# Kernel optimization log

Hardware: AMD Instinct MI355X
Metric: run time of the kernel (lower is better)

## Reference

```python
import jax, jax.numpy as jnp
import numpy as np

EPS = 1e-6

def setup_inputs() -> dict:
    key = jax.random.key(0)
    ks = jax.random.split(key, 8)
    S, B, I, D, L = 1024, 16, 1024, 1024, 2
    std = np.sqrt(2.0 / (5.0 * I))
    inp = {
        "input": jax.random.normal(ks[0], (S, B, I), jnp.float32),
        "h0": jnp.zeros((L, B, D), jnp.float32),
        "extra0": jnp.zeros((L, B, 3 * D), jnp.float32),
        "W0": jax.random.normal(ks[1], (4 * D, I), jnp.float32) * std,
        "b0": jnp.zeros((4 * D,), jnp.float32).at[2 * D:3 * D].set(
            jax.random.uniform(ks[2], (D,), jnp.float32, 3.0, 6.0)),
        "r0": jnp.zeros((4 * D,), jnp.float32),
        "W1": jax.random.normal(ks[3], (4 * D, D), jnp.float32) * std,
        "b1": jnp.zeros((4 * D,), jnp.float32).at[2 * D:3 * D].set(
            jax.random.uniform(ks[4], (D,), jnp.float32, 3.0, 6.0)),
        "r1": jnp.zeros((4 * D,), jnp.float32),
    }
    return inp

def _cell(x, c, n, h, m, W, b, r):
    # x: (B, in), states: (B, D), W: (4D, in), b/r: (4D,)
    D = h.shape[-1]
    pre = x @ W.T + b  # (B, 4D)
    rz, ri, rf, ro = jnp.split(r, 4)
    z_pre = pre[:, 0 * D:1 * D] + rz * h
    i_pre = pre[:, 1 * D:2 * D] + ri * h
    f_pre = pre[:, 2 * D:3 * D] + rf * h
    o_pre = pre[:, 3 * D:4 * D] + ro * h
    z_t = jnp.tanh(z_pre)
    o_t = jax.nn.sigmoid(o_pre)
    m_new = jnp.maximum(f_pre + m, i_pre)
    f_t = jnp.exp(f_pre + m - m_new)
    i_t = jnp.exp(i_pre - m_new)
    c_new = f_t * c + i_t * z_t
    n_new = f_t * n + i_t
    h_new = o_t * (c_new / (jnp.abs(n_new) + EPS))
    return h_new, c_new, n_new, m_new

def _run(input, h0, extra0, params):
    D = h0.shape[-1]
    c0 = extra0[:, :, 0 * D:1 * D]
    n0 = extra0[:, :, 1 * D:2 * D]
    m0 = extra0[:, :, 2 * D:3 * D]

    def step(carry, x_t):
        h, c, n, m = carry  # each (L, B, D)
        x = x_t
        hs, cs, ns, ms = [], [], [], []
        for l, (W, b, r) in enumerate(params):
            h_new, c_new, n_new, m_new = _cell(x, c[l], n[l], h[l], m[l], W, b, r)
            hs.append(h_new); cs.append(c_new); ns.append(n_new); ms.append(m_new)
            x = h_new
        carry = (jnp.stack(hs), jnp.stack(cs), jnp.stack(ns), jnp.stack(ms))
        return carry, x

    (h_f, c_f, n_f, m_f), output = jax.lax.scan(step, (h0, c0, n0, m0), input)
    extra_f = jnp.concatenate([c_f, n_f, m_f], axis=-1)
    return output, h_f, extra_f

def reference(input, h0, extra0, W0, b0, r0, W1, b1, r1):
    params = [(W0, b0, r0), (W1, b1, r1)]
    return _run(input, h0, extra0, params)
```

## Files before the change

### kernel.cpp

```cpp
#include <hip/hip_runtime.h>
#include <hip/hip_bf16.h>

#define S_LEN  1024
#define BATCH  16
#define IDIM   1024
#define DDIM   1024
#define NG     4096
#define BD     16384
#define LAYERS 2
#define PF     16

typedef __attribute__((ext_vector_type(8))) short   short8;
typedef __attribute__((ext_vector_type(4))) float   floatx4;
typedef __attribute__((address_space(1))) void      as1_void;
typedef __attribute__((address_space(3))) void      as3_void;

#define L2E  1.4426950408889634f
#define LN2  0.6931471805599453f

#define EXP2F(x) exp2f(x)

static __device__ __forceinline__ unsigned short f2bf(float x) {
    unsigned int u = __float_as_uint(x);
    return (unsigned short)((u + 0x7fffu + ((u >> 16) & 1u)) >> 16);
}

__global__ void detect_dtype(const void* w, int* flag)
{
    const __hip_bfloat16* p = (const __hip_bfloat16*)w;
    float mx = 0.0f;
    for (int i = threadIdx.x; i < 4096; i += 64) {
        float v = __bfloat162float(p[i]);
        float a = fabsf(v);
        if (!(a == a)) a = 1e30f;
        mx = fmaxf(mx, a);
    }
#pragma unroll
    for (int o = 32; o > 0; o >>= 1)
        mx = fmaxf(mx, __shfl_down(mx, o, 64));
    if (threadIdx.x == 0) *flag = (mx > 1e3f) ? 1 : 0;
}

__global__ void detect_rzero(const float* __restrict__ pb, int* __restrict__ rflag)
{
    const float* r = pb + (size_t)(1 + 2 * blockIdx.x) * NG;
    int nz = 0;
    for (int i = threadIdx.x; i < NG; i += 256) nz |= (r[i] != 0.0f);
    __shared__ int s[4];
    const int w = threadIdx.x >> 6;
    const int any = __any(nz) ? 1 : 0;
    if ((threadIdx.x & 63) == 0) s[w] = any;
    __syncthreads();
    if (threadIdx.x == 0) rflag[blockIdx.x] = !(s[0] | s[1] | s[2] | s[3]);
}

__global__ void to_bf16(const void* src, size_t elem_off, const int* flag,
                        unsigned short* dst, int n)
{
    const int i = blockIdx.x * 256 + threadIdx.x;
    if (i >= n) return;
    if (*flag) dst[i] = f2bf(((const float*)src)[elem_off + i]);
    else       dst[i] = ((const unsigned short*)src)[elem_off + i];
}

__global__ void to_f32(const void* src, const int* flag, float* dst, int n)
{
    const int i = blockIdx.x * 256 + threadIdx.x;
    if (i >= n) return;
    dst[i] = (*flag) ? ((const float*)src)[i]
                     : __bfloat162float(((const __hip_bfloat16*)src)[i]);
}

__global__ __launch_bounds__(256, 2)
void gemm_bias(const __hip_bfloat16* __restrict__ A,
               const __hip_bfloat16* __restrict__ W,
               const float* __restrict__ bias,
               unsigned short* __restrict__ out,
               const int* __restrict__ rflag)
{
    constexpr int K = 1024;
    __shared__ alignas(16) __hip_bfloat16 sA[128 * 32];
    __shared__ alignas(16) __hip_bfloat16 sB[128 * 32];

    const int t  = threadIdx.x;
    const int m0 = blockIdx.y * 128;
    const int nb = blockIdx.x;
    const int lr = t & 15;
    const int q  = (t >> 4) & 3;
    const int w  = t >> 6;
    const int wm = w >> 1, wn = w & 1;
    const int sr = t >> 2;
    const int qd = t & 3;
    const int qs = qd ^ ((sr >> 1) & 3);

    floatx4 acc[4][4] = {};

    const __hip_bfloat16* Ab = A + (size_t)(m0 + sr) * K + qs * 8;
    const int wrow = ((sr >> 5) << 10) + nb * 32 + (sr & 31);
    const __hip_bfloat16* Wb = W + (size_t)wrow * K + qs * 8;

    const int rc = (q ^ ((lr >> 1) & 3)) * 8;

    for (int k0 = 0; k0 < K; k0 += 32) {
        __syncthreads();
        __builtin_amdgcn_global_load_lds((as1_void*)(Ab + k0),            (as3_void*)&sA[sr * 32 + qd * 8],        16, 0, 0);
        __builtin_amdgcn_global_load_lds((as1_void*)(Ab + 64 * K + k0),   (as3_void*)&sA[(sr + 64) * 32 + qd * 8], 16, 0, 0);
        __builtin_amdgcn_global_load_lds((as1_void*)(Wb + k0),            (as3_void*)&sB[sr * 32 + qd * 8],        16, 0, 0);
        __builtin_amdgcn_global_load_lds((as1_void*)(Wb + 2048 * K + k0), (as3_void*)&sB[(sr + 64) * 32 + qd * 8], 16, 0, 0);
        __syncthreads();

        short8 af[4], bf[4];
#pragma unroll
        for (int i = 0; i < 4; i++)
            af[i] = *(const short8*)&sA[(wm * 64 + i * 16 + lr) * 32 + rc];
#pragma unroll
        for (int j = 0; j < 4; j++)
            bf[j] = *(const short8*)&sB[(j * 32 + wn * 16 + lr) * 32 + rc];
#pragma unroll
        for (int i = 0; i < 4; i++)
#pragma unroll
            for (int j = 0; j < 4; j++)
                acc[i][j] = __builtin_amdgcn_mfma_f32_16x16x32_bf16(af[i], bf[j], acc[i][j], 0, 0, 0);
    }

    const int d = nb * 32 + wn * 16 + lr;
    const float sc[4] = {2.0f * L2E, L2E, L2E, L2E};
    float bb[4];
#pragma unroll
    for (int g = 0; g < 4; g++) bb[g] = sc[g] * bias[g * 1024 + d];

    const int rfast = *rflag;

#pragma unroll
    for (int i = 0; i < 4; i++) {
#pragma unroll
        for (int reg = 0; reg < 4; reg++) {
            const int row = m0 + wm * 64 + i * 16 + q * 4 + reg;
            float v[4];
#pragma unroll
            for (int g = 0; g < 4; g++)
                v[g] = acc[i][g][reg] * sc[g] + bb[g];
            if (rfast) {
                const float zv = v[0];
                const float e2 = EXP2F(-fabsf(zv));
                v[0] = copysignf((1.0f - e2) * __builtin_amdgcn_rcpf(1.0f + e2), zv);
                v[3] = __builtin_amdgcn_rcpf(1.0f + EXP2F(-v[3]));
            }
            union { unsigned short us[4]; uint2 u2; } pk;
#pragma unroll
            for (int g = 0; g < 4; g++) pk.us[g] = f2bf(v[g]);
            *(uint2*)(out + (size_t)row * NG + d * 4) = pk.u2;
        }
    }
}

template<int MODE>
__global__ void slstm_scan(const unsigned int* __restrict__ pre,
                           const float* __restrict__ r,
                           float* __restrict__ state,
                           unsigned short* __restrict__ hseq,
                           void* __restrict__ gout, size_t gout_eoff,
                           const int* __restrict__ flag,
                           const int* __restrict__ rflag, int T)
{
    const int idx = blockIdx.x * 64 + threadIdx.x;
    const int b = idx >> 10;
    const int d = idx & 1023;
    const int fl = *flag;
    const int rfast = *rflag;

    const float rz = r[d]            * (2.0f * L2E);
    const float ri = r[DDIM + d]     * L2E;
    const float rf = r[2 * DDIM + d] * L2E;
    const float ro = r[3 * DDIM + d] * L2E;

    float c  = state[0 * BD + idx];
    float n  = state[1 * BD + idx];
    float m2 = state[2 * BD + idx];
    float h  = state[3 * BD + idx];

    const size_t stp = 32768;
    const unsigned int* p = pre + (size_t)b * 2048 + (size_t)d * 2;

    unsigned short* hb = hseq + (size_t)b * DDIM + d;
    float*          fo = (float*)gout + gout_eoff + (size_t)b * DDIM + d;
    unsigned short* bo = (unsigned short*)gout + gout_eoff + (size_t)b * DDIM + d;

    unsigned int k0[PF], k1[PF];
#pragma unroll
    for (int u = 0; u < PF; u++) {
        const uint2 v = *(const uint2*)(p + (size_t)u * stp);
        k0[u] = v.x; k1[u] = v.y;
    }

    if (rfast) {
        for (int t8 = 0; t8 < T; t8 += PF) {
#pragma unroll
            for (int u = 0; u < PF; u++) {
                const float zt = __uint_as_float(k0[u] << 16);
                const float i2 = __uint_as_float(k0[u] & 0xffff0000u);
                const float f2 = __uint_as_float(k1[u] << 16);
                const float ot = __uint_as_float(k1[u] & 0xffff0000u);

                const uint2 nv = *(const uint2*)(p + (size_t)(t8 + u + PF) * stp);
                k0[u] = nv.x; k1[u] = nv.y;

                const float fm = f2 + m2;
                const float mn = fmaxf(fm, i2);
                const float ft = EXP2F(fm - mn);
                const float it = EXP2F(i2 - mn);

                c  = fmaf(ft, c, it * zt);
                n  = fmaf(ft, n, it);
                m2 = mn;
                h  = ot * c * __builtin_amdgcn_rcpf(fabsf(n) + 1e-6f);

                const size_t toff = (size_t)(t8 + u) * BD;
                if (MODE == 0)      hb[toff] = f2bf(h);
                else if (fl)        fo[toff] = h;
                else                bo[toff] = f2bf(h);
            }
        }
    } else {
        for (int t8 = 0; t8 < T; t8 += PF) {
#pragma unroll
            for (int u = 0; u < PF; u++) {
                float z2 = __uint_as_float(k0[u] << 16);
                float i2 = __uint_as_float(k0[u] & 0xffff0000u);
                float f2 = __uint_as_float(k1[u] << 16);
                float o2 = __uint_as_float(k1[u] & 0xffff0000u);

                const uint2 nv = *(const uint2*)(p + (size_t)(t8 + u + PF) * stp);
                k0[u] = nv.x; k1[u] = nv.y;

                z2 = fmaf(rz, h, z2);
                i2 = fmaf(ri, h, i2);
                f2 = fmaf(rf, h, f2);
                o2 = fmaf(ro, h, o2);

                const float fm = f2 + m2;
                const float mn = fmaxf(fm, i2);
                const float ft = EXP2F(fm - mn);
                const float it = EXP2F(i2 - mn);

                const float e2 = EXP2F(-fabsf(z2));
                const float zt = copysignf((1.0f - e2) * __builtin_amdgcn_rcpf(1.0f + e2), z2);
                const float ot = __builtin_amdgcn_rcpf(1.0f + EXP2F(-o2));

                c  = ft * c + it * zt;
                n  = ft * n + it;
                m2 = mn;
                h  = ot * c * __builtin_amdgcn_rcpf(fabsf(n) + 1e-6f);

                const size_t toff = (size_t)(t8 + u) * BD;
                if (MODE == 0)      hb[toff] = f2bf(h);
                else if (fl)        fo[toff] = h;
                else                bo[toff] = f2bf(h);
            }
        }
    }

    state[0 * BD + idx] = c;
    state[1 * BD + idx] = n;
    state[2 * BD + idx] = m2;
    state[3 * BD + idx] = h;
}

__global__ void init_state(const void* __restrict__ h0,
                           const void* __restrict__ extra0,
                           const int* __restrict__ flag,
                           float* __restrict__ state)
{
    const int idx = blockIdx.x * 256 + threadIdx.x;
    const int l  = idx / BD;
    const int bd = idx % BD;
    const int b = bd >> 10, d = bd & 1023;
    float* st = state + (size_t)l * 4 * BD;
    const size_t eoff = ((size_t)l * BATCH + b) * (3 * DDIM);
    float cv, nv, mv, hv;
    if (*flag) {
        const float* e = (const float*)extra0 + eoff;
        cv = e[d]; nv = e[DDIM + d]; mv = e[2 * DDIM + d];
        hv = ((const float*)h0)[(size_t)l * BD + bd];
    } else {
        const __hip_bfloat16* e = (const __hip_bfloat16*)extra0 + eoff;
        cv = __bfloat162float(e[d]);
        nv = __bfloat162float(e[DDIM + d]);
        mv = __bfloat162float(e[2 * DDIM + d]);
        hv = __bfloat162float(((const __hip_bfloat16*)h0)[(size_t)l * BD + bd]);
    }
    st[0 * BD + bd] = cv;
    st[1 * BD + bd] = nv;
    st[2 * BD + bd] = mv * L2E;
    st[3 * BD + bd] = hv;
}

__global__ void finalize(const float* __restrict__ state,
                         void* __restrict__ out,
                         const int* __restrict__ flag)
{
    const int idx = blockIdx.x * 256 + threadIdx.x;
    const int l  = idx / BD;
    const int bd = idx % BD;
    const int b = bd >> 10, d = bd & 1023;
    const float* st = state + (size_t)l * 4 * BD;
    const float cv = st[0 * BD + bd], nv = st[1 * BD + bd];
    const float mv = st[2 * BD + bd] * LN2;
    const float hv = st[3 * BD + bd];

    const size_t hoff = (size_t)S_LEN * BD + idx;
    const size_t eoff = (size_t)S_LEN * BD + (size_t)LAYERS * BD
                      + ((size_t)l * BATCH + b) * (3 * DDIM);
    if (*flag) {
        float* o = (float*)out;
        o[hoff] = hv;
        o[eoff + d] = cv; o[eoff + DDIM + d] = nv; o[eoff + 2 * DDIM + d] = mv;
    } else {
        unsigned short* o = (unsigned short*)out;
        o[hoff] = f2bf(hv);
        o[eoff + d]            = f2bf(cv);
        o[eoff + DDIM + d]     = f2bf(nv);
        o[eoff + 2 * DDIM + d] = f2bf(mv);
    }
}

__global__ void zero_out_k(void* __restrict__ out, const int* __restrict__ flag,
                           int out_size)
{
    const size_t i = (size_t)blockIdx.x * 256 + threadIdx.x;
    const size_t nb = (size_t)out_size * ((*flag) ? 4 : 2);
    char* o = (char*)out;
    for (size_t j = i * 4; j < (i + 1) * 4 && j < nb; j++) o[j] = 0;
}

extern "C" void kernel_launch(void* const* d_in, const int* in_sizes, int n_in,
                              void* d_out, int out_size, void* d_ws, size_t ws_size,
                              hipStream_t stream)
{
    const void* input  = d_in[0];
    const void* h0     = d_in[1];
    const void* extra0 = d_in[2];
    const void* W0     = d_in[3];
    const void* b0     = d_in[4];
    const void* r0     = d_in[5];
    const void* W1     = d_in[6];
    const void* b1     = d_in[7];
    const void* r1     = d_in[8];

    const size_t FLAG_B  = 256;
    const size_t STATE_B = (size_t)LAYERS * 4 * BD * 4;
    const size_t W_B     = (size_t)NG * IDIM * 2;
    const size_t PB_B    = (size_t)4 * NG * 4;
    const size_t FIXED   = FLAG_B + STATE_B + 2 * W_B + PB_B;

    int T = 0;
    for (int cand = S_LEN; cand >= 8; cand >>= 1) {
        size_t need = FIXED
                    + (size_t)cand * BD * 2
                    + (size_t)cand * BD * 2
                    + (size_t)(cand + PF) * BATCH * NG * 2;
        if (need <= ws_size) { T = cand; break; }
    }

    char* ws = (char*)d_ws;
    int*   flag  = (int*)ws;
    int*   rflag = flag + 1;
    float* state = (float*)(ws + FLAG_B);
    __hip_bfloat16* W0b = (__hip_bfloat16*)(ws + FLAG_B + STATE_B);
    __hip_bfloat16* W1b = W0b + (size_t)NG * IDIM;
    float* pb    = (float*)(ws + FLAG_B + STATE_B + 2 * W_B);
    float* b0f = pb, *r0f = pb + NG, *b1f = pb + 2 * NG, *r1f = pb + 3 * NG;
    unsigned short* Ain  = (unsigned short*)(ws + FIXED);
    unsigned short* hseq = Ain + (size_t)T * BD;
    unsigned short* pre  = hseq + (size_t)T * BD;

    detect_dtype<<<dim3(1), dim3(64), 0, stream>>>(W0, flag);

    if (T == 0) {
        zero_out_k<<<dim3((out_size + 255) / 256), dim3(256), 0, stream>>>(d_out, flag, out_size);
        return;
    }

    const int WN = NG * IDIM;
    to_bf16<<<dim3(WN / 256), dim3(256), 0, stream>>>(W0, 0, flag, (unsigned short*)W0b, WN);
    to_bf16<<<dim3(WN / 256), dim3(256), 0, stream>>>(W1, 0, flag, (unsigned short*)W1b, WN);
    to_f32<<<dim3(NG / 256), dim3(256), 0, stream>>>(b0, flag, b0f, NG);
    to_f32<<<dim3(NG / 256), dim3(256), 0, stream>>>(r0, flag, r0f, NG);
    to_f32<<<dim3(NG / 256), dim3(256), 0, stream>>>(b1, flag, b1f, NG);
    to_f32<<<dim3(NG / 256), dim3(256), 0, stream>>>(r1, flag, r1f, NG);

    detect_rzero<<<dim3(2), dim3(256), 0, stream>>>(pb, rflag);

    init_state<<<dim3(LAYERS * BD / 256), dim3(256), 0, stream>>>(h0, extra0, flag, state);

    const dim3 gemmGrid(32, (T * BATCH) / 128);
    const dim3 scanGrid(BD / 64);
    const int  nch = S_LEN / T;

    for (int ch = 0; ch < nch; ch++) {
        const int t0 = ch * T;

        to_bf16<<<dim3((T * BD) / 256), dim3(256), 0, stream>>>(
            input, (size_t)t0 * BD, flag, Ain, T * BD);

        gemm_bias<<<gemmGrid, 256, 0, stream>>>((const __hip_bfloat16*)Ain, W0b, b0f, pre, rflag + 0);
        slstm_scan<0><<<scanGrid, 64, 0, stream>>>((const unsigned int*)pre, r0f, state,
                                                   hseq, (void*)0, 0, flag, rflag + 0, T);
        gemm_bias<<<gemmGrid, 256, 0, stream>>>((const __hip_bfloat16*)hseq, W1b, b1f, pre, rflag + 1);
        slstm_scan<1><<<scanGrid, 64, 0, stream>>>((const unsigned int*)pre, r1f,
                                                   state + 4 * BD, (unsigned short*)0,
                                                   d_out, (size_t)t0 * BD, flag, rflag + 1, T);
    }

    finalize<<<dim3(LAYERS * BD / 256), dim3(256), 0, stream>>>(state, d_out, flag);
}
```

Before: 686.1 us.

## Fuse small prep kernels, cap chunk length, drop LDS swizzle, raise prefetch

Merges the bias/recurrent conversion, zero-recurrence detection and state initialisation into one prep kernel to cut launches. Caps the time-chunk length at 256 so the sequence runs as several chunks, and doubles the prefetch distance PF used in the scan. Removes the XOR swizzle from the GEMM's LDS tile layout, which simplifies addressing but may bring back LDS bank conflicts. The shorter chunks add per-chunk launches, while the pre buffer stays smaller and more cache-friendly.

```diff
diff --git a/kernel.cpp b/kernel.cpp
--- a/kernel.cpp
+++ b/kernel.cpp
@@ -8,7 +8,8 @@
 #define NG     4096
 #define BD     16384
 #define LAYERS 2
-#define PF     16
+#define PF     32
+#define TMAX   256
 
 typedef __attribute__((ext_vector_type(8))) short   short8;
 typedef __attribute__((ext_vector_type(4))) float   floatx4;
@@ -41,19 +42,6 @@
     if (threadIdx.x == 0) *flag = (mx > 1e3f) ? 1 : 0;
 }
 
-__global__ void detect_rzero(const float* __restrict__ pb, int* __restrict__ rflag)
-{
-    const float* r = pb + (size_t)(1 + 2 * blockIdx.x) * NG;
-    int nz = 0;
-    for (int i = threadIdx.x; i < NG; i += 256) nz |= (r[i] != 0.0f);
-    __shared__ int s[4];
-    const int w = threadIdx.x >> 6;
-    const int any = __any(nz) ? 1 : 0;
-    if ((threadIdx.x & 63) == 0) s[w] = any;
-    __syncthreads();
-    if (threadIdx.x == 0) rflag[blockIdx.x] = !(s[0] | s[1] | s[2] | s[3]);
-}
-
 __global__ void to_bf16(const void* src, size_t elem_off, const int* flag,
                         unsigned short* dst, int n)
 {
@@ -63,12 +51,71 @@
     else       dst[i] = ((const unsigned short*)src)[elem_off + i];
 }
 
-__global__ void to_f32(const void* src, const int* flag, float* dst, int n)
-{
-    const int i = blockIdx.x * 256 + threadIdx.x;
-    if (i >= n) return;
-    dst[i] = (*flag) ? ((const float*)src)[i]
-                     : __bfloat162float(((const __hip_bfloat16*)src)[i]);
+__global__ void prep_small(const void* __restrict__ h0,
+                           const void* __restrict__ extra0,
+                           const void* __restrict__ b0s, const void* __restrict__ r0s,
+                           const void* __restrict__ b1s, const void* __restrict__ r1s,
+                           const int* __restrict__ flag,
+                           float* __restrict__ state,
+                           float* __restrict__ pb,
+                           int* __restrict__ rflag)
+{
+    const int blk = blockIdx.x;
+    const int fl = *flag;
+
+    if (blk < 128) {
+        const int idx = blk * 256 + threadIdx.x;
+        const int l  = idx / BD;
+        const int bd = idx % BD;
+        const int b = bd >> 10, d = bd & 1023;
+        float* st = state + (size_t)l * 4 * BD;
+        const size_t eoff = ((size_t)l * BATCH + b) * (3 * DDIM);
+        float cv, nv, mv, hv;
+        if (fl) {
+            const float* e = (const float*)extra0 + eoff;
+            cv = e[d]; nv = e[DDIM + d]; mv = e[2 * DDIM + d];
+            hv = ((const float*)h0)[(size_t)l * BD + bd];
+        } else {
+            const __hip_bfloat16* e = (const __hip_bfloat16*)extra0 + eoff;
+            cv = __bfloat162float(e[d]);
+            nv = __bfloat162float(e[DDIM + d]);
+            mv = __bfloat162float(e[2 * DDIM + d]);
+            hv = __bfloat162float(((const __hip_bfloat16*)h0)[(size_t)l * BD + bd]);
+        }
+        st[0 * BD + bd] = cv;
+        st[1 * BD + bd] = nv;
+        st[2 * BD + bd] = mv * L2E;
+        st[3 * BD + bd] = hv;
+        return;
+    }
+
+    const int which = blk - 128;
+    const void* src = (which == 0) ? b0s : (which == 1) ? r0s
+                    : (which == 2) ? b1s : r1s;
+    float* dst = pb + (size_t)which * NG;
+    int nz = 0;
+#pragma unroll
+    for (int j = 0; j < NG / 256; j++) {
+        const int i = j * 256 + threadIdx.x;
+        float v;
+        if (fl) {
+            v = ((const float*)src)[i];
+            nz |= (v != 0.0f);
+        } else {
+            const unsigned short u = ((const unsigned short*)src)[i];
+            nz |= ((u & 0x7fffu) != 0);
+            v = __bfloat162float(((const __hip_bfloat16*)src)[i]);
+        }
+        dst[i] = v;
+    }
+    if (which == 1 || which == 3) {
+        __shared__ int s[4];
+        const int w = threadIdx.x >> 6;
+        const int any = __any(nz) ? 1 : 0;
+        if ((threadIdx.x & 63) == 0) s[w] = any;
+        __syncthreads();
+        if (threadIdx.x == 0) rflag[which >> 1] = !(s[0] | s[1] | s[2] | s[3]);
+    }
 }
 
 __global__ __launch_bounds__(256, 2)
@@ -90,32 +137,29 @@
     const int w  = t >> 6;
     const int wm = w >> 1, wn = w & 1;
     const int sr = t >> 2;
-    const int qd = t & 3;
-    const int qs = qd ^ ((sr >> 1) & 3);
+    const int sk = (t & 3) * 8;
 
     floatx4 acc[4][4] = {};
 
-    const __hip_bfloat16* Ab = A + (size_t)(m0 + sr) * K + qs * 8;
+    const __hip_bfloat16* Ab = A + (size_t)(m0 + sr) * K + sk;
     const int wrow = ((sr >> 5) << 10) + nb * 32 + (sr & 31);
-    const __hip_bfloat16* Wb = W + (size_t)wrow * K + qs * 8;
-
-    const int rc = (q ^ ((lr >> 1) & 3)) * 8;
+    const __hip_bfloat16* Wb = W + (size_t)wrow * K + sk;
 
     for (int k0 = 0; k0 < K; k0 += 32) {
         __syncthreads();
-        __builtin_amdgcn_global_load_lds((as1_void*)(Ab + k0),            (as3_void*)&sA[sr * 32 + qd * 8],        16, 0, 0);
-        __builtin_amdgcn_global_load_lds((as1_void*)(Ab + 64 * K + k0),   (as3_void*)&sA[(sr + 64) * 32 + qd * 8], 16, 0, 0);
-        __builtin_amdgcn_global_load_lds((as1_void*)(Wb + k0),            (as3_void*)&sB[sr * 32 + qd * 8],        16, 0, 0);
-        __builtin_amdgcn_global_load_lds((as1_void*)(Wb + 2048 * K + k0), (as3_void*)&sB[(sr + 64) * 32 + qd * 8], 16, 0, 0);
+        __builtin_amdgcn_global_load_lds((as1_void*)(Ab + k0),            (as3_void*)&sA[sr * 32 + sk],        16, 0, 0);
+        __builtin_amdgcn_global_load_lds((as1_void*)(Ab + 64 * K + k0),   (as3_void*)&sA[(sr + 64) * 32 + sk], 16, 0, 0);
+        __builtin_amdgcn_global_load_lds((as1_void*)(Wb + k0),            (as3_void*)&sB[sr * 32 + sk],        16, 0, 0);
+        __builtin_amdgcn_global_load_lds((as1_void*)(Wb + 2048 * K + k0), (as3_void*)&sB[(sr + 64) * 32 + sk], 16, 0, 0);
         __syncthreads();
 
         short8 af[4], bf[4];
 #pragma unroll
         for (int i = 0; i < 4; i++)
-            af[i] = *(const short8*)&sA[(wm * 64 + i * 16 + lr) * 32 + rc];
+            af[i] = *(const short8*)&sA[(wm * 64 + i * 16 + lr) * 32 + q * 8];
 #pragma unroll
         for (int j = 0; j < 4; j++)
-            bf[j] = *(const short8*)&sB[(j * 32 + wn * 16 + lr) * 32 + rc];
+            bf[j] = *(const short8*)&sB[(j * 32 + wn * 16 + lr) * 32 + q * 8];
 #pragma unroll
         for (int i = 0; i < 4; i++)
 #pragma unroll
@@ -264,35 +308,6 @@
     state[1 * BD + idx] = n;
     state[2 * BD + idx] = m2;
     state[3 * BD + idx] = h;
-}
-
-__global__ void init_state(const void* __restrict__ h0,
-                           const void* __restrict__ extra0,
-                           const int* __restrict__ flag,
-                           float* __restrict__ state)
-{
-    const int idx = blockIdx.x * 256 + threadIdx.x;
-    const int l  = idx / BD;
-    const int bd = idx % BD;
-    const int b = bd >> 10, d = bd & 1023;
-    float* st = state + (size_t)l * 4 * BD;
-    const size_t eoff = ((size_t)l * BATCH + b) * (3 * DDIM);
-    float cv, nv, mv, hv;
-    if (*flag) {
-        const float* e = (const float*)extra0 + eoff;
-        cv = e[d]; nv = e[DDIM + d]; mv = e[2 * DDIM + d];
-        hv = ((const float*)h0)[(size_t)l * BD + bd];
-    } else {
-        const __hip_bfloat16* e = (const __hip_bfloat16*)extra0 + eoff;
-        cv = __bfloat162float(e[d]);
-        nv = __bfloat162float(e[DDIM + d]);
-        mv = __bfloat162float(e[2 * DDIM + d]);
-        hv = __bfloat162float(((const __hip_bfloat16*)h0)[(size_t)l * BD + bd]);
-    }
-    st[0 * BD + bd] = cv;
-    st[1 * BD + bd] = nv;
-    st[2 * BD + bd] = mv * L2E;
-    st[3 * BD + bd] = hv;
 }
 
 __global__ void finalize(const float* __restrict__ state,
@@ -354,7 +369,7 @@
     const size_t FIXED   = FLAG_B + STATE_B + 2 * W_B + PB_B;
 
     int T = 0;
-    for (int cand = S_LEN; cand >= 8; cand >>= 1) {
+    for (int cand = TMAX; cand >= PF; cand >>= 1) {
         size_t need = FIXED
                     + (size_t)cand * BD * 2
                     + (size_t)cand * BD * 2
@@ -384,14 +399,9 @@
     const int WN = NG * IDIM;
     to_bf16<<<dim3(WN / 256), dim3(256), 0, stream>>>(W0, 0, flag, (unsigned short*)W0b, WN);
     to_bf16<<<dim3(WN / 256), dim3(256), 0, stream>>>(W1, 0, flag, (unsigned short*)W1b, WN);
-    to_f32<<<dim3(NG / 256), dim3(256), 0, stream>>>(b0, flag, b0f, NG);
-    to_f32<<<dim3(NG / 256), dim3(256), 0, stream>>>(r0, flag, r0f, NG);
-    to_f32<<<dim3(NG / 256), dim3(256), 0, stream>>>(b1, flag, b1f, NG);
-    to_f32<<<dim3(NG / 256), dim3(256), 0, stream>>>(r1, flag, r1f, NG);
-
-    detect_rzero<<<dim3(2), dim3(256), 0, stream>>>(pb, rflag);
-
-    init_state<<<dim3(LAYERS * BD / 256), dim3(256), 0, stream>>>(h0, extra0, flag, state);
+
+    prep_small<<<dim3(132), dim3(256), 0, stream>>>(h0, extra0, b0, r0, b1, r1,
+                                                    flag, state, pb, rflag);
 
     const dim3 gemmGrid(32, (T * BATCH) / 128);
     const dim3 scanGrid(BD / 64);
```

Measured after the change: 804.7 us. 17.3% more time.
